# Performance work log

Hardware: AMD Instinct MI355X
Metric: run time of the kernel (lower is better)

## Reference

```python
import jax, jax.numpy as jnp
import numpy as np

NUM_OUT_EDGES = 2
NUM_INTERMEDIATE = 2
NUM_FSM_STATES = NUM_OUT_EDGES + NUM_INTERMEDIATE  # S = 4
NUM_EDGE_TYPES = 3
NUM_VARIANTS = 4
NUM_NODE_TYPES = 8
NUM_NODES = 256
BACKTRACK_FAILS_PROB = 0.001
EDGE_PROB = 0.05  # avg degree ~ 12.8 per edge type


def setup_inputs() -> dict:
    key = jax.random.key(0)
    k1, k2, k3, k4 = jax.random.split(key, 4)
    vw = jax.random.uniform(k1, (NUM_NODES, NUM_NODES, NUM_VARIANTS))
    vw = vw / jnp.sum(vw, axis=-1, keepdims=True)  # nonneg, sums to 1 on last axis
    adjacency = (jax.random.uniform(k2, (NUM_EDGE_TYPES, NUM_NODES, NUM_NODES)) < EDGE_PROB).astype(jnp.float32)
    n_actions = NUM_EDGE_TYPES * NUM_FSM_STATES + 3  # moves + ACCEPT/BACKTRACK/FAIL
    log_routing_params = 0.5 * jax.random.normal(
        k3, (NUM_VARIANTS, NUM_NODE_TYPES, NUM_FSM_STATES, n_actions))
    node_types = jax.random.randint(k4, (NUM_NODES,), 0, NUM_NODE_TYPES)
    return {
        'variant_weights': vw,
        'adjacency': adjacency,
        'log_routing_params': log_routing_params,
        'node_types': node_types,
        'steps': 48,
    }


def _forward(variant_weights, adjacency, log_routing_params, node_types, steps):
    N = variant_weights.shape[0]
    S, T, E = NUM_FSM_STATES, NUM_EDGE_TYPES, NUM_OUT_EDGES
    dt = variant_weights.dtype

    # Row-normalized per-edge-type adjacency (uniform over typed successors;
    deg = jnp.sum(adjacency, axis=-1, keepdims=True)
    a_norm = adjacency / jnp.maximum(deg, 1.0)  # [T, N, N]

    # routing_softmax over actions; policy conditioned on (variant, node type, fsm state)
    policy = jax.nn.softmax(log_routing_params, axis=-1)  # [V, NT, S, A]
    pol_n = policy[:, node_types]                          # [V, N, S, A]

    # Mix policy variants per (start node i, current node j)
    mixed = jnp.einsum('ijv,vjsa->ijsa', variant_weights, pol_n)  # [N, N, S, A]
    p_move = mixed[..., :T * S].reshape(N, N, S, T, S)  # MOVE(edge type t, next state u)
    p_accept = mixed[..., T * S]                        # ACCEPT at current node
    p_back = mixed[..., T * S + 1]                      # BACKTRACK to start node

    # Start states: edge type e starts in fsm state e at node i (one-hot).
    eyeS = jnp.eye(S, dtype=dt)[:E]  # [E, S]
    eyeN = jnp.eye(N, dtype=dt)      # [N, N]
    dist0 = eyeS[:, None, :, None] * eyeN[None, :, None, :]  # [E, N, S, N]
    restart = dist0 * (1.0 - BACKTRACK_FAILS_PROB)

    def step(carry, _):
        dist, accept = carry  # dist: [E, N_start, S, N_cur], accept: [E, N, N]
        accept = accept + jnp.einsum('eisj,ijs->eij', dist, p_accept)
        back = jnp.einsum('eisj,ijs->ei', dist, p_back)
        tmp = jnp.einsum('eisj,ijstu->eituj', dist, p_move)   # pick edge type + next state
        moved = jnp.einsum('eituj,tjk->eiuk', tmp, a_norm)    # move along typed edges
        dist = moved + back[:, :, None, None] * restart
        return (dist, accept), None

    accept0 = jnp.zeros((E, N, N), dt)
    (dist, accept), _ = jax.lax.scan(step, (dist0, accept0), None, length=steps)
    # absorb remaining accept probability after final transition
    accept = accept + jnp.einsum('eisj,ijs->eij', dist, p_accept)
    return accept  # [num_out_edges, num_nodes, num_nodes]


def reference(variant_weights, adjacency, log_routing_params, node_types, steps):
    return _forward(variant_weights, adjacency, log_routing_params, node_types, steps)
```

## Files before the change

kernel.cpp:

```cpp
#include <hip/hip_runtime.h>
#include <hip/hip_fp16.h>

#define NN    256
#define SS    4
#define TT    3
#define VV    4
#define NTY   8
#define NAC   15
#define CAPG  48
#define CAPE  (CAPG * 2)
#define ROWB  40
#define ZROWB (NN * ROWB)
#define BUFB  (ZROWB + ROWB)
#define ZPK   ((unsigned)ZROWB | ((unsigned)ZROWB << 16))
#define GMAXR 32

typedef _Float16 h2v __attribute__((ext_vector_type(2)));

#if defined(__has_builtin)
#if __has_builtin(__builtin_amdgcn_fdot2)
#define HAVE_FDOT2 1
#endif
#endif

static __device__ __forceinline__ unsigned ph2(float a, float b) {
    union { __half2 h; unsigned u; } c;
    c.h = __floats2half2_rn(a, b);
    return c.u;
}
static __device__ __forceinline__ h2v bch2(unsigned u) {
    union { unsigned u; h2v h; } c; c.u = u; return c.h;
}
static __device__ __forceinline__ float2 h2f2(unsigned u) {
    union { unsigned u; __half2 h; } c; c.u = u; return __half22float2(c.h);
}

__global__ void k_setup(const float* __restrict__ adj,
                        const float* __restrict__ lrp,
                        float* __restrict__ inv_deg,
                        float* __restrict__ pol,
                        unsigned* __restrict__ epk,
                        int* __restrict__ gcnt) {
    const int b = blockIdx.x;
    const int tid = threadIdx.x;

    if (b < TT * NN) {
        __shared__ float wsum[4];
        float s = adj[(size_t)b * NN + tid];
#pragma unroll
        for (int off = 32; off > 0; off >>= 1) s += __shfl_down(s, off, 64);
        if ((tid & 63) == 0) wsum[tid >> 6] = s;
        __syncthreads();
        if (tid == 0)
            inv_deg[b] = 1.0f / fmaxf(wsum[0] + wsum[1] + wsum[2] + wsum[3], 1.0f);
    } else if (b < TT * NN + NN) {
        __shared__ int cnt;
        __shared__ unsigned short offs[CAPE + 2];
        const int col = b - TT * NN;
        if (tid == 0) cnt = 0;
        __syncthreads();
#pragma unroll
        for (int t = 0; t < TT; t++) {
            float a = adj[((size_t)t * NN + tid) * NN + col];
            if (a != 0.f) {
                int idx = atomicAdd(&cnt, 1);
                if (idx < CAPE) offs[idx] = (unsigned short)(tid * ROWB + t * 8);
            }
        }
        __syncthreads();
        int c = cnt; if (c > CAPE) c = CAPE;
        if (tid == 0 && (c & 1)) offs[c] = (unsigned short)ZROWB;
        __syncthreads();
        const int g = (c + 1) >> 1;
        for (int gg = tid; gg < g; gg += blockDim.x)
            epk[(size_t)gg * NN + col] =
                (unsigned)offs[2 * gg] | ((unsigned)offs[2 * gg + 1] << 16);
        if (tid == 0) gcnt[col] = g;
    } else {
        if (tid < VV * NTY * SS) {
            float x[NAC]; float m = -3.4e38f;
#pragma unroll
            for (int a = 0; a < NAC; a++) { x[a] = lrp[tid * NAC + a]; m = fmaxf(m, x[a]); }
            float ssum = 0.f;
#pragma unroll
            for (int a = 0; a < NAC; a++) { x[a] = __expf(x[a] - m); ssum += x[a]; }
            float inv = 1.f / ssum;
#pragma unroll
            for (int a = 0; a < NAC; a++) pol[tid * NAC + a] = x[a] * inv;
        }
    }
}

__global__ __launch_bounds__(256, 2) void k_main(
    const float* __restrict__ vw,
    const int* __restrict__ node_types,
    const float* __restrict__ pol,
    const float* __restrict__ inv_deg,
    const unsigned* __restrict__ epk,
    const int* __restrict__ gcnt,
    const int* __restrict__ steps_p,
    float* __restrict__ out)
{
    const int i    = blockIdx.x & 255;
    const int e    = blockIdx.x >> 8;
    const int col  = threadIdx.x;
    const int wv   = col >> 6;
    const int lane = col & 63;
    const int steps = steps_p[0];

    __shared__ __align__(16) char tmpb[2 * BUFB];
    __shared__ float backp[2][4];

    if (col < 20) {
        int pb = col / 10, w = col % 10;
        ((unsigned*)(tmpb + pb * BUFB + ZROWB))[w] = 0u;
    }

    const float4 w4 = *(const float4*)(vw + ((size_t)i * NN + col) * VV);
    const float wvv[VV] = {w4.x, w4.y, w4.z, w4.w};
    const int ntj = node_types[col];
    float pmS[SS][12], pacc[SS], pback[SS];
#pragma unroll
    for (int s = 0; s < SS; s++) {
        pacc[s] = 0.f; pback[s] = 0.f;
#pragma unroll
        for (int a = 0; a < 12; a++) pmS[s][a] = 0.f;
    }
#pragma unroll
    for (int v = 0; v < VV; v++) {
        const float* pr = pol + (size_t)(v * NTY + ntj) * SS * NAC;
#pragma unroll
        for (int s = 0; s < SS; s++) {
            const float* p = pr + s * NAC;
#pragma unroll
            for (int a = 0; a < 12; a++) pmS[s][a] = fmaf(wvv[v], p[a], pmS[s][a]);
            pacc[s]  = fmaf(wvv[v], p[12], pacc[s]);
            pback[s] = fmaf(wvv[v], p[13], pback[s]);
        }
    }
    {
        float invd[TT];
#pragma unroll
        for (int t = 0; t < TT; t++) invd[t] = inv_deg[t * NN + col];
#pragma unroll
        for (int s = 0; s < SS; s++)
#pragma unroll
            for (int a = 0; a < 12; a++) pmS[s][a] *= invd[a >> 2];
    }

    float D0 = (0 == e && col == i) ? 1.f : 0.f;
    float D1 = (1 == e && col == i) ? 1.f : 0.f;
    float D2 = 0.f, D3 = 0.f;
    float acc = 0.f;

    const int g_all = gcnt[col];
    int gm = g_all;
#pragma unroll
    for (int off = 32; off > 0; off >>= 1) {
        int o = __shfl_xor(gm, off, 64);
        gm = o > gm ? o : gm;
    }
    const int gmax = __builtin_amdgcn_readfirstlane(gm);

    unsigned ep[GMAXR];
#pragma unroll
    for (int g = 0; g < GMAXR; g++) {
        unsigned pk = epk[(size_t)g * NN + col];
        ep[g] = (g < g_all) ? pk : ZPK;
    }

    const h2v S10 = {(_Float16)1.0f, (_Float16)0.0f};
    const h2v S01 = {(_Float16)0.0f, (_Float16)1.0f};
    char* const myrow0 = tmpb + col * ROWB;

    for (int step = 0; step < steps; step++) {
        const int par = step & 1;
        char* const buf = tmpb + par * BUFB;

        float ad = D0 * pacc[0];
        ad = fmaf(D1, pacc[1], ad); ad = fmaf(D2, pacc[2], ad); ad = fmaf(D3, pacc[3], ad);
        acc += ad;
        float bj = D0 * pback[0];
        bj = fmaf(D1, pback[1], bj); bj = fmaf(D2, pback[2], bj); bj = fmaf(D3, pback[3], bj);

        float tv[12];
#pragma unroll
        for (int a = 0; a < 12; a++) {
            float x = D0 * pmS[0][a];
            x = fmaf(D1, pmS[1][a], x);
            x = fmaf(D2, pmS[2][a], x);
            x = fmaf(D3, pmS[3][a], x);
            tv[a] = x;
        }
        char* const myrow = myrow0 + par * BUFB;
        uint2 wA; wA.x = ph2(tv[0], tv[1]);  wA.y = ph2(tv[2],  tv[3]);
        uint2 wB; wB.x = ph2(tv[4], tv[5]);  wB.y = ph2(tv[6],  tv[7]);
        uint2 wC; wC.x = ph2(tv[8], tv[9]);  wC.y = ph2(tv[10], tv[11]);
        *(uint2*)(myrow)      = wA;
        *(uint2*)(myrow + 8)  = wB;
        *(uint2*)(myrow + 16) = wC;

#pragma unroll
        for (int off = 32; off > 0; off >>= 1) bj += __shfl_down(bj, off, 64);
        if (lane == 0) backp[par][wv] = bj;

        __syncthreads();

        float d0a = 0.f, d1a = 0.f, d2a = 0.f, d3a = 0.f;
        float d0b = 0.f, d1b = 0.f, d2b = 0.f, d3b = 0.f;
#pragma unroll
        for (int g = 0; g < GMAXR; g++) {
            if (g < gmax) {
                const unsigned pk = ep[g];
                const uint2 q0 = *(const uint2*)(buf + (pk & 0xffffu));
                const uint2 q1 = *(const uint2*)(buf + (pk >> 16));
#ifdef HAVE_FDOT2
                if (g & 1) {
                    d0b = __builtin_amdgcn_fdot2(bch2(q0.x), S10, d0b, false);
                    d1b = __builtin_amdgcn_fdot2(bch2(q0.x), S01, d1b, false);
                    d2b = __builtin_amdgcn_fdot2(bch2(q0.y), S10, d2b, false);
                    d3b = __builtin_amdgcn_fdot2(bch2(q0.y), S01, d3b, false);
                    d0b = __builtin_amdgcn_fdot2(bch2(q1.x), S10, d0b, false);
                    d1b = __builtin_amdgcn_fdot2(bch2(q1.x), S01, d1b, false);
                    d2b = __builtin_amdgcn_fdot2(bch2(q1.y), S10, d2b, false);
                    d3b = __builtin_amdgcn_fdot2(bch2(q1.y), S01, d3b, false);
                } else {
                    d0a = __builtin_amdgcn_fdot2(bch2(q0.x), S10, d0a, false);
                    d1a = __builtin_amdgcn_fdot2(bch2(q0.x), S01, d1a, false);
                    d2a = __builtin_amdgcn_fdot2(bch2(q0.y), S10, d2a, false);
                    d3a = __builtin_amdgcn_fdot2(bch2(q0.y), S01, d3a, false);
                    d0a = __builtin_amdgcn_fdot2(bch2(q1.x), S10, d0a, false);
                    d1a = __builtin_amdgcn_fdot2(bch2(q1.x), S01, d1a, false);
                    d2a = __builtin_amdgcn_fdot2(bch2(q1.y), S10, d2a, false);
                    d3a = __builtin_amdgcn_fdot2(bch2(q1.y), S01, d3a, false);
                }
#else
                float2 f0 = h2f2(q0.x), f1 = h2f2(q0.y), f2 = h2f2(q1.x), f3 = h2f2(q1.y);
                if (g & 1) {
                    d0b += f0.x + f2.x; d1b += f0.y + f2.y;
                    d2b += f1.x + f3.x; d3b += f1.y + f3.y;
                } else {
                    d0a += f0.x + f2.x; d1a += f0.y + f2.y;
                    d2a += f1.x + f3.x; d3a += f1.y + f3.y;
                }
#endif
            }
        }
        for (int g = GMAXR; g < gmax; g++) {
            unsigned pk = epk[(size_t)g * NN + col];
            pk = (g < g_all) ? pk : ZPK;
            const uint2 q0 = *(const uint2*)(buf + (pk & 0xffffu));
            const uint2 q1 = *(const uint2*)(buf + (pk >> 16));
            float2 f0 = h2f2(q0.x), f1 = h2f2(q0.y), f2 = h2f2(q1.x), f3 = h2f2(q1.y);
            d0a += f0.x + f2.x; d1a += f0.y + f2.y;
            d2a += f1.x + f3.x; d3a += f1.y + f3.y;
        }

        float d0 = d0a + d0b, d1 = d1a + d1b, d2 = d2a + d2b, d3 = d3a + d3b;

        if (col == i) {
            const float* bp = backp[par];
            float back = bp[0] + bp[1] + bp[2] + bp[3];
            if (e == 0) d0 = fmaf(back, 0.999f, d0);
            else        d1 = fmaf(back, 0.999f, d1);
        }
        D0 = d0; D1 = d1; D2 = d2; D3 = d3;
    }

    float ad = D0 * pacc[0];
    ad = fmaf(D1, pacc[1], ad); ad = fmaf(D2, pacc[2], ad); ad = fmaf(D3, pacc[3], ad);
    acc += ad;
    out[((size_t)e * NN + i) * NN + col] = acc;
}

extern "C" void kernel_launch(void* const* d_in, const int* in_sizes, int n_in,
                              void* d_out, int out_size, void* d_ws, size_t ws_size,
                              hipStream_t stream) {
    const float* vw  = (const float*)d_in[0];
    const float* adj = (const float*)d_in[1];
    const float* lrp = (const float*)d_in[2];
    const int* node_types = (const int*)d_in[3];
    const int* steps_p    = (const int*)d_in[4];

    float* ws       = (float*)d_ws;
    float* pol      = ws;
    float* inv_deg  = ws + 1920;
    int*   gcnt     = (int*)(ws + 2688);
    unsigned* epk   = (unsigned*)(ws + 2944);

    k_setup<<<TT * NN + NN + 1, 256, 0, stream>>>(adj, lrp, inv_deg, pol, epk, gcnt);
    k_main<<<2 * NN, 256, 0, stream>>>(vw, node_types, pol, inv_deg, epk, gcnt,
                                       steps_p, (float*)d_out);
}
```

Before: 184.6 us.

## Split each destination column across two threads and batch CSC build by four columns

The main kernel now uses 512 threads per block, two per destination column. Each thread handles half of the move actions and half of the incoming edge groups, and the partial sums are combined with a lane shuffle. This halves the per-thread serial gather chain and register footprint so more waves can hide LDS latency, at the cost of extra shuffles and duplicated state updates. The setup kernel also builds the edge lists for four columns per block using float4 loads, cutting the number of setup blocks.

Result: faster. 166.6 us (-9.8%).

```diff
diff --git a/kernel.cpp b/kernel.cpp
--- a/kernel.cpp
+++ b/kernel.cpp
@@ -13,7 +13,7 @@
 #define ZROWB (NN * ROWB)
 #define BUFB  (ZROWB + ROWB)
 #define ZPK   ((unsigned)ZROWB | ((unsigned)ZROWB << 16))
-#define GMAXR 32
+#define GMR   16
 
 typedef _Float16 h2v __attribute__((ext_vector_type(2)));
 
@@ -53,29 +53,35 @@
         __syncthreads();
         if (tid == 0)
             inv_deg[b] = 1.0f / fmaxf(wsum[0] + wsum[1] + wsum[2] + wsum[3], 1.0f);
-    } else if (b < TT * NN + NN) {
-        __shared__ int cnt;
-        __shared__ unsigned short offs[CAPE + 2];
-        const int col = b - TT * NN;
-        if (tid == 0) cnt = 0;
+    } else if (b < TT * NN + 64) {
+        __shared__ int cnt[4];
+        __shared__ unsigned short offs[4][CAPE + 2];
+        const int c4 = (b - TT * NN) * 4;
+        if (tid < 4) cnt[tid] = 0;
         __syncthreads();
 #pragma unroll
         for (int t = 0; t < TT; t++) {
-            float a = adj[((size_t)t * NN + tid) * NN + col];
-            if (a != 0.f) {
-                int idx = atomicAdd(&cnt, 1);
-                if (idx < CAPE) offs[idx] = (unsigned short)(tid * ROWB + t * 8);
+            const float4 a4 = *(const float4*)(adj + ((size_t)t * NN + tid) * NN + c4);
+            const float av[4] = {a4.x, a4.y, a4.z, a4.w};
+#pragma unroll
+            for (int c = 0; c < 4; c++) {
+                if (av[c] != 0.f) {
+                    int idx = atomicAdd(&cnt[c], 1);
+                    if (idx < CAPE) offs[c][idx] = (unsigned short)(tid * ROWB + t * 8);
+                }
             }
         }
         __syncthreads();
-        int c = cnt; if (c > CAPE) c = CAPE;
-        if (tid == 0 && (c & 1)) offs[c] = (unsigned short)ZROWB;
-        __syncthreads();
-        const int g = (c + 1) >> 1;
-        for (int gg = tid; gg < g; gg += blockDim.x)
-            epk[(size_t)gg * NN + col] =
-                (unsigned)offs[2 * gg] | ((unsigned)offs[2 * gg + 1] << 16);
-        if (tid == 0) gcnt[col] = g;
+        const int c    = tid >> 6;
+        const int lane = tid & 63;
+        int cc = cnt[c]; if (cc > CAPE) cc = CAPE;
+        if (lane == 0 && (cc & 1)) offs[c][cc] = (unsigned short)ZROWB;
+        __syncthreads();
+        const int g = (cc + 1) >> 1;
+        for (int gg = lane; gg < g; gg += 64)
+            epk[(size_t)gg * NN + (c4 + c)] =
+                (unsigned)offs[c][2 * gg] | ((unsigned)offs[c][2 * gg + 1] << 16);
+        if (lane == 0) gcnt[c4 + c] = g;
     } else {
         if (tid < VV * NTY * SS) {
             float x[NAC]; float m = -3.4e38f;
@@ -91,7 +97,7 @@
     }
 }
 
-__global__ __launch_bounds__(256, 2) void k_main(
+__global__ __launch_bounds__(512, 4) void k_main(
     const float* __restrict__ vw,
     const int* __restrict__ node_types,
     const float* __restrict__ pol,
@@ -103,28 +109,31 @@
 {
     const int i    = blockIdx.x & 255;
     const int e    = blockIdx.x >> 8;
-    const int col  = threadIdx.x;
-    const int wv   = col >> 6;
-    const int lane = col & 63;
+    const int tid  = threadIdx.x;
+    const int col  = tid >> 1;
+    const int h    = tid & 1;
+    const int lane = tid & 63;
+    const int wv   = tid >> 6;
     const int steps = steps_p[0];
 
     __shared__ __align__(16) char tmpb[2 * BUFB];
-    __shared__ float backp[2][4];
-
-    if (col < 20) {
-        int pb = col / 10, w = col % 10;
+    __shared__ __align__(16) float backp[2][8];
+
+    if (tid < 20) {
+        int pb = tid / 10, w = tid % 10;
         ((unsigned*)(tmpb + pb * BUFB + ZROWB))[w] = 0u;
     }
 
     const float4 w4 = *(const float4*)(vw + ((size_t)i * NN + col) * VV);
     const float wvv[VV] = {w4.x, w4.y, w4.z, w4.w};
     const int ntj = node_types[col];
-    float pmS[SS][12], pacc[SS], pback[SS];
+    const int ab  = h * 6;
+    float pm6[SS][6], pcb[SS];
 #pragma unroll
     for (int s = 0; s < SS; s++) {
-        pacc[s] = 0.f; pback[s] = 0.f;
-#pragma unroll
-        for (int a = 0; a < 12; a++) pmS[s][a] = 0.f;
+        pcb[s] = 0.f;
+#pragma unroll
+        for (int a = 0; a < 6; a++) pm6[s][a] = 0.f;
     }
 #pragma unroll
     for (int v = 0; v < VV; v++) {
@@ -133,9 +142,8 @@
         for (int s = 0; s < SS; s++) {
             const float* p = pr + s * NAC;
 #pragma unroll
-            for (int a = 0; a < 12; a++) pmS[s][a] = fmaf(wvv[v], p[a], pmS[s][a]);
-            pacc[s]  = fmaf(wvv[v], p[12], pacc[s]);
-            pback[s] = fmaf(wvv[v], p[13], pback[s]);
+            for (int a = 0; a < 6; a++) pm6[s][a] = fmaf(wvv[v], p[ab + a], pm6[s][a]);
+            pcb[s] = fmaf(wvv[v], p[12 + h], pcb[s]);
         }
     }
     {
@@ -145,7 +153,7 @@
 #pragma unroll
         for (int s = 0; s < SS; s++)
 #pragma unroll
-            for (int a = 0; a < 12; a++) pmS[s][a] *= invd[a >> 2];
+            for (int a = 0; a < 6; a++) pm6[s][a] *= invd[(ab + a) >> 2];
     }
 
     float D0 = (0 == e && col == i) ? 1.f : 0.f;
@@ -154,51 +162,48 @@
     float acc = 0.f;
 
     const int g_all = gcnt[col];
-    int gm = g_all;
+    const int ch = (g_all - h + 1) >> 1;
+    int km = ch;
 #pragma unroll
     for (int off = 32; off > 0; off >>= 1) {
-        int o = __shfl_xor(gm, off, 64);
-        gm = o > gm ? o : gm;
-    }
-    const int gmax = __builtin_amdgcn_readfirstlane(gm);
-
-    unsigned ep[GMAXR];
-#pragma unroll
-    for (int g = 0; g < GMAXR; g++) {
-        unsigned pk = epk[(size_t)g * NN + col];
-        ep[g] = (g < g_all) ? pk : ZPK;
+        int o = __shfl_xor(km, off, 64);
+        km = o > km ? o : km;
+    }
+    const int kmax = __builtin_amdgcn_readfirstlane(km);
+
+    unsigned ep[GMR];
+#pragma unroll
+    for (int k = 0; k < GMR; k++) {
+        unsigned pk = epk[(size_t)(2 * k + h) * NN + col];
+        ep[k] = (2 * k + h < g_all) ? pk : ZPK;
     }
 
     const h2v S10 = {(_Float16)1.0f, (_Float16)0.0f};
     const h2v S01 = {(_Float16)0.0f, (_Float16)1.0f};
-    char* const myrow0 = tmpb + col * ROWB;
+    char* const myrow0 = tmpb + col * ROWB + h * 12;
 
     for (int step = 0; step < steps; step++) {
         const int par = step & 1;
         char* const buf = tmpb + par * BUFB;
 
-        float ad = D0 * pacc[0];
-        ad = fmaf(D1, pacc[1], ad); ad = fmaf(D2, pacc[2], ad); ad = fmaf(D3, pacc[3], ad);
-        acc += ad;
-        float bj = D0 * pback[0];
-        bj = fmaf(D1, pback[1], bj); bj = fmaf(D2, pback[2], bj); bj = fmaf(D3, pback[3], bj);
-
-        float tv[12];
-#pragma unroll
-        for (int a = 0; a < 12; a++) {
-            float x = D0 * pmS[0][a];
-            x = fmaf(D1, pmS[1][a], x);
-            x = fmaf(D2, pmS[2][a], x);
-            x = fmaf(D3, pmS[3][a], x);
+        float r4 = D0 * pcb[0];
+        r4 = fmaf(D1, pcb[1], r4); r4 = fmaf(D2, pcb[2], r4); r4 = fmaf(D3, pcb[3], r4);
+        if (h == 0) acc += r4;
+        float bj = h ? r4 : 0.f;
+
+        float tv[6];
+#pragma unroll
+        for (int a = 0; a < 6; a++) {
+            float x = D0 * pm6[0][a];
+            x = fmaf(D1, pm6[1][a], x);
+            x = fmaf(D2, pm6[2][a], x);
+            x = fmaf(D3, pm6[3][a], x);
             tv[a] = x;
         }
         char* const myrow = myrow0 + par * BUFB;
-        uint2 wA; wA.x = ph2(tv[0], tv[1]);  wA.y = ph2(tv[2],  tv[3]);
-        uint2 wB; wB.x = ph2(tv[4], tv[5]);  wB.y = ph2(tv[6],  tv[7]);
-        uint2 wC; wC.x = ph2(tv[8], tv[9]);  wC.y = ph2(tv[10], tv[11]);
-        *(uint2*)(myrow)      = wA;
-        *(uint2*)(myrow + 8)  = wB;
-        *(uint2*)(myrow + 16) = wC;
+        *(unsigned*)(myrow)     = ph2(tv[0], tv[1]);
+        *(unsigned*)(myrow + 4) = ph2(tv[2], tv[3]);
+        *(unsigned*)(myrow + 8) = ph2(tv[4], tv[5]);
 
 #pragma unroll
         for (int off = 32; off > 0; off >>= 1) bj += __shfl_down(bj, off, 64);
@@ -209,13 +214,13 @@
         float d0a = 0.f, d1a = 0.f, d2a = 0.f, d3a = 0.f;
         float d0b = 0.f, d1b = 0.f, d2b = 0.f, d3b = 0.f;
 #pragma unroll
-        for (int g = 0; g < GMAXR; g++) {
-            if (g < gmax) {
-                const unsigned pk = ep[g];
+        for (int k = 0; k < GMR; k++) {
+            if (k < kmax) {
+                const unsigned pk = ep[k];
                 const uint2 q0 = *(const uint2*)(buf + (pk & 0xffffu));
                 const uint2 q1 = *(const uint2*)(buf + (pk >> 16));
 #ifdef HAVE_FDOT2
-                if (g & 1) {
+                if (k & 1) {
                     d0b = __builtin_amdgcn_fdot2(bch2(q0.x), S10, d0b, false);
                     d1b = __builtin_amdgcn_fdot2(bch2(q0.x), S01, d1b, false);
                     d2b = __builtin_amdgcn_fdot2(bch2(q0.y), S10, d2b, false);
@@ -236,7 +241,7 @@
                 }
 #else
                 float2 f0 = h2f2(q0.x), f1 = h2f2(q0.y), f2 = h2f2(q1.x), f3 = h2f2(q1.y);
-                if (g & 1) {
+                if (k & 1) {
                     d0b += f0.x + f2.x; d1b += f0.y + f2.y;
                     d2b += f1.x + f3.x; d3b += f1.y + f3.y;
                 } else {
@@ -246,9 +251,9 @@
 #endif
             }
         }
-        for (int g = GMAXR; g < gmax; g++) {
-            unsigned pk = epk[(size_t)g * NN + col];
-            pk = (g < g_all) ? pk : ZPK;
+        for (int k = GMR; k < kmax; k++) {
+            unsigned pk = epk[(size_t)(2 * k + h) * NN + col];
+            pk = (2 * k + h < g_all) ? pk : ZPK;
             const uint2 q0 = *(const uint2*)(buf + (pk & 0xffffu));
             const uint2 q1 = *(const uint2*)(buf + (pk >> 16));
             float2 f0 = h2f2(q0.x), f1 = h2f2(q0.y), f2 = h2f2(q1.x), f3 = h2f2(q1.y);
@@ -258,19 +263,28 @@
 
         float d0 = d0a + d0b, d1 = d1a + d1b, d2 = d2a + d2b, d3 = d3a + d3b;
 
+        d0 += __shfl_xor(d0, 1, 64);
+        d1 += __shfl_xor(d1, 1, 64);
+        d2 += __shfl_xor(d2, 1, 64);
+        d3 += __shfl_xor(d3, 1, 64);
+
+        const float4 b0 = *(const float4*)(&backp[par][0]);
+        const float4 b1 = *(const float4*)(&backp[par][4]);
+        const float back = ((b0.x + b0.y) + (b0.z + b0.w)) +
+                           ((b1.x + b1.y) + (b1.z + b1.w));
         if (col == i) {
-            const float* bp = backp[par];
-            float back = bp[0] + bp[1] + bp[2] + bp[3];
             if (e == 0) d0 = fmaf(back, 0.999f, d0);
             else        d1 = fmaf(back, 0.999f, d1);
         }
         D0 = d0; D1 = d1; D2 = d2; D3 = d3;
     }
 
-    float ad = D0 * pacc[0];
-    ad = fmaf(D1, pacc[1], ad); ad = fmaf(D2, pacc[2], ad); ad = fmaf(D3, pacc[3], ad);
-    acc += ad;
-    out[((size_t)e * NN + i) * NN + col] = acc;
+    float r4 = D0 * pcb[0];
+    r4 = fmaf(D1, pcb[1], r4); r4 = fmaf(D2, pcb[2], r4); r4 = fmaf(D3, pcb[3], r4);
+    if (h == 0) {
+        acc += r4;
+        out[((size_t)e * NN + i) * NN + col] = acc;
+    }
 }
 
 extern "C" void kernel_launch(void* const* d_in, const int* in_sizes, int n_in,
@@ -288,7 +302,7 @@
     int*   gcnt     = (int*)(ws + 2688);
     unsigned* epk   = (unsigned*)(ws + 2944);
 
-    k_setup<<<TT * NN + NN + 1, 256, 0, stream>>>(adj, lrp, inv_deg, pol, epk, gcnt);
-    k_main<<<2 * NN, 256, 0, stream>>>(vw, node_types, pol, inv_deg, epk, gcnt,
+    k_setup<<<TT * NN + 64 + 1, 256, 0, stream>>>(adj, lrp, inv_deg, pol, epk, gcnt);
+    k_main<<<2 * NN, 512, 0, stream>>>(vw, node_types, pol, inv_deg, epk, gcnt,
                                        steps_p, (float*)d_out);
 }
```
